# Kernel tuning notes

Measured on AMD Instinct MI355X. Metric: run time of the kernel, lower is better.

Reference implementation:

```python
import jax, jax.numpy as jnp
import numpy as np

B, F, O = 32, 26, 20
IN, G = 2048, 512
REL = 53
EPS = 1e-5  # BatchNorm1d default eps


def setup_inputs() -> dict:
    key = jax.random.key(0)
    ks = jax.random.split(key, 10)
    inp = {
        "region_feats": jax.random.normal(ks[0], (B, F, O, IN), jnp.float32),
        "region_masks": jnp.ones((B, F, O), jnp.float32),
        "rel_feats": jax.random.randint(ks[1], (B, F, O, O), 0, REL, jnp.int64),
        "tem_feats": jax.random.uniform(ks[2], (B, F * O, F * O), jnp.float32),
        # learned params (eval mode: dropout off, BN uses running stats)
        "rel_W": jax.random.normal(ks[3], (G, IN), jnp.float32) * (1.0 / np.sqrt(IN)),
        "rel_b": jnp.zeros((G,), jnp.float32),
        "rel_emb": jax.random.normal(ks[4], (REL, G), jnp.float32) * 0.02,
        "tem_W": jax.random.normal(ks[5], (G, IN), jnp.float32) * (1.0 / np.sqrt(IN)),
        "tem_b": jnp.zeros((G,), jnp.float32),
        "bn_w": jnp.ones((F * O,), jnp.float32),
        "bn_b": jnp.zeros((F * O,), jnp.float32),
        "bn_rm": jnp.zeros((F * O,), jnp.float32),
        "bn_rv": jnp.ones((F * O,), jnp.float32),
    }
    return inp


def reference(region_feats, region_masks, rel_feats, tem_feats,
              rel_W, rel_b, rel_emb, tem_W, tem_b,
              bn_w, bn_b, bn_rm, bn_rv):
    b, f, o, _ = region_feats.shape
    # ---- RELATIONAL FEATURE GRAPH ----
    # [B,F,O,G]
    rel_region = jnp.einsum("bfoi,gi->bfog", region_feats, rel_W) + rel_b
    # embedding lookup: [B,F,O,O,G]
    emb = rel_emb[rel_feats]
    mask = (rel_feats > 0).astype(region_feats.dtype)  # [B,F,O,O]
    msum = jnp.sum(mask, axis=3)                        # [B,F,O]
    # sum_j mask_ij * emb_ij  (masked reduction over neighbor dim)
    emb_sum = jnp.einsum("bfijg,bfij->bfig", emb, mask)
    # sum_j mask_ij * r_i == r_i * msum_i, so (emb_sum + r*msum)/msum
    rel_out = (emb_sum + rel_region * msum[..., None]) / msum[..., None]
    rel_out = rel_out.reshape(b, f * o, -1)
    # ---- TEMPORAL FEATURE GRAPH ----
    tem_region = jnp.einsum("bfoi,gi->bfog", region_feats, tem_W) + tem_b
    tem_region = tem_region.reshape(b, f * o, -1)
    tem_sum = jnp.sum(tem_feats, axis=2)                # [B, F*O]
    tem_out = jnp.matmul(tem_feats, tem_region) / tem_sum[..., None]
    # ---- OUTPUT ----
    out = jnp.concatenate([rel_out, tem_out], axis=-1)  # [B, F*O, 2G]
    out = jnp.tanh(out)
    # BatchNorm1d over channel dim 1 (eval mode, running stats)
    inv = bn_w / jnp.sqrt(bn_rv + EPS)                  # [F*O]
    out = (out - bn_rm[None, :, None]) * inv[None, :, None] + bn_b[None, :, None]
    return out
```

## Files before the change

### kernel.cpp

```cpp
#include <hip/hip_runtime.h>
#include <stdint.h>

#define BB 32
#define FO 520
#define M1 16640
#define KIN 2048
#define KA 2112
#define N1 1024
#define GG 512
#define K2P 576
#define M2 640

typedef unsigned short u16;
typedef short v8s __attribute__((ext_vector_type(8)));
typedef float v4f __attribute__((ext_vector_type(4)));

__device__ __forceinline__ u16 f2bf(float f) {
  union { float f; unsigned u; } v; v.f = f;
  unsigned r = v.u + 0x7fffu + ((v.u >> 16) & 1u);
  return (u16)(r >> 16);
}

__device__ __forceinline__ float fast_tanh(float x) {
  float cx = fminf(fmaxf(x, -15.f), 15.f);
  float e = __expf(2.f * cx);
  return (e - 1.f) / (e + 1.f);
}

__global__ void prep_all_kernel(const float* __restrict__ rf, const int* __restrict__ rel,
                                const float* __restrict__ relW, const float* __restrict__ temW,
                                const float* __restrict__ emb, const float* __restrict__ tem,
                                u16* __restrict__ A1, u16* __restrict__ Wc,
                                u16* __restrict__ A2, float* __restrict__ tsum) {
  const int blk = blockIdx.x;
  const int t = threadIdx.x;
  if (blk < M1 + 1024) {
    const float* src;
    u16* orow;
    if (blk < M1) { src = rf + (size_t)blk * KIN; orow = A1 + (size_t)blk * KA; }
    else {
      const int n = blk - M1;
      src = (n < GG) ? (relW + (size_t)n * KIN) : (temW + (size_t)(n - GG) * KIN);
      orow = Wc + (size_t)n * KA;
    }
    const float4* p = (const float4*)src;
    float4 a = p[2 * t], b = p[2 * t + 1];
    v8s v;
    v[0] = (short)f2bf(a.x); v[1] = (short)f2bf(a.y);
    v[2] = (short)f2bf(a.z); v[3] = (short)f2bf(a.w);
    v[4] = (short)f2bf(b.x); v[5] = (short)f2bf(b.y);
    v[6] = (short)f2bf(b.z); v[7] = (short)f2bf(b.w);
    *(v8s*)(orow + t * 8) = v;
    if (t < 64) {
      float sval = 0.f;
      if (blk < M1) {
        const int* rp = rel + (size_t)blk * 20;
        int cnt = 0, ms = 0;
#pragma unroll
        for (int j = 0; j < 20; ++j) { int ix = rp[j]; cnt += (ix == t + 1); ms += (ix > 0); }
        if (t < 52 && ms > 0) sval = (float)cnt / (float)ms;
      } else {
        const int n = blk - M1;
        if (n < GG && t < 52) sval = emb[(size_t)(t + 1) * GG + n];
      }
      orow[KIN + t] = f2bf(sval);
    }
    return;
  }
  const int w = t >> 6, l = t & 63;
  const int row = (blk - (M1 + 1024)) * 4 + w;
  const int b = row / M2, i = row % M2;
  u16* orow = A2 + (size_t)row * K2P;
  v8s z = {0, 0, 0, 0, 0, 0, 0, 0};
  if (i >= FO) {
    *(v8s*)(orow + l * 8) = z;
    if (l < 8) *(v8s*)(orow + (64 + l) * 8) = z;
    return;
  }
  const float* srow = tem + ((size_t)b * FO + i) * FO;
  float s = 0.f;
  {
    float4 a = *(const float4*)(srow + 8 * l);
    float4 bb = *(const float4*)(srow + 8 * l + 4);
    s += a.x + a.y + a.z + a.w + bb.x + bb.y + bb.z + bb.w;
    v8s v;
    v[0] = (short)f2bf(a.x); v[1] = (short)f2bf(a.y);
    v[2] = (short)f2bf(a.z); v[3] = (short)f2bf(a.w);
    v[4] = (short)f2bf(bb.x); v[5] = (short)f2bf(bb.y);
    v[6] = (short)f2bf(bb.z); v[7] = (short)f2bf(bb.w);
    *(v8s*)(orow + l * 8) = v;
  }
  if (l < 8) {
    if (l == 0) {
      float4 a = *(const float4*)(srow + 512);
      float4 bb = *(const float4*)(srow + 516);
      s += a.x + a.y + a.z + a.w + bb.x + bb.y + bb.z + bb.w;
      v8s v;
      v[0] = (short)f2bf(a.x); v[1] = (short)f2bf(a.y);
      v[2] = (short)f2bf(a.z); v[3] = (short)f2bf(a.w);
      v[4] = (short)f2bf(bb.x); v[5] = (short)f2bf(bb.y);
      v[6] = (short)f2bf(bb.z); v[7] = (short)f2bf(bb.w);
      *(v8s*)(orow + 512) = v;
    } else {
      *(v8s*)(orow + (64 + l) * 8) = z;
    }
  }
#pragma unroll
  for (int off = 32; off > 0; off >>= 1) s += __shfl_down(s, off);
  if (l == 0) tsum[(size_t)b * FO + i] = s;
}

#define G1_STAGE(DST)                                                                            \
  do {                                                                                           \
    u16* dst_ = smem + (DST);                                                                    \
    __builtin_amdgcn_global_load_lds((const __attribute__((address_space(1))) void*)ga0,         \
        (__attribute__((address_space(3))) void*)(dst_ + lofA0), 16, 0, 0);                      \
    __builtin_amdgcn_global_load_lds((const __attribute__((address_space(1))) void*)ga1,         \
        (__attribute__((address_space(3))) void*)(dst_ + lofA1), 16, 0, 0);                      \
    __builtin_amdgcn_global_load_lds((const __attribute__((address_space(1))) void*)gb0,         \
        (__attribute__((address_space(3))) void*)(dst_ + lofB0), 16, 0, 0);                      \
    ga0 += 32; ga1 += 32; gb0 += 32;                                                             \
  } while (0)

#define G1_COMPUTE(CB)                                                                           \
  do {                                                                                           \
    const u16* As_ = smem + (CB) * 12288;                                                        \
    const u16* Bs_ = As_ + 8192;                                                                 \
    v8s af[4], bf[4];                                                                            \
    _Pragma("unroll") for (int t4 = 0; t4 < 4; ++t4) {                                           \
      const int ra = wm * 64 + t4 * 16 + r16;                                                    \
      const int rb = wn * 64 + t4 * 16 + r16;                                                    \
      af[t4] = *(const v8s*)&As_[ra * 32 + ((quad ^ ((ra >> 1) & 3)) * 8)];                      \
      bf[t4] = *(const v8s*)&Bs_[rb * 32 + ((quad ^ ((rb >> 1) & 3)) * 8)];                      \
    }                                                                                            \
    _Pragma("unroll") for (int mtt = 0; mtt < 4; ++mtt)                                          \
      _Pragma("unroll") for (int ntt = 0; ntt < 4; ++ntt)                                        \
        acc[mtt][ntt] =                                                                          \
            __builtin_amdgcn_mfma_f32_16x16x32_bf16(af[mtt], bf[ntt], acc[mtt][ntt], 0, 0, 0);   \
  } while (0)

__global__ __launch_bounds__(512, 4) void gemm1_kernel(
    const u16* __restrict__ A, const u16* __restrict__ Wc,
    const float* __restrict__ rel_b, const float* __restrict__ tem_b,
    const float* __restrict__ bn_w, const float* __restrict__ bn_b,
    const float* __restrict__ bn_rm, const float* __restrict__ bn_rv,
    float* __restrict__ out, u16* __restrict__ BT) {
  __shared__ u16 smem[36864];
  const int tid = threadIdx.x;
  const int lane = tid & 63;
  const int wv = tid >> 6, wm = wv >> 1, wn = wv & 1;
  const int id = blockIdx.x;
  const int wgid = (id & 7) * 65 + (id >> 3);
  const int mt = wgid >> 3, nt = wgid & 7;
  const int m0 = mt * 256, n0 = nt * 128;
  const int quad = lane >> 4, r16 = lane & 15;

  const u16 *ga0, *ga1, *gb0;
  {
    const int r0 = tid >> 2, sl0 = tid & 3;
    ga0 = A + (size_t)(m0 + r0) * KA + (sl0 ^ ((r0 >> 1) & 3)) * 8;
    const int r1 = 128 + (tid >> 2);
    ga1 = A + (size_t)(m0 + r1) * KA + (sl0 ^ ((r1 >> 1) & 3)) * 8;
    gb0 = Wc + (size_t)(n0 + r0) * KA + (sl0 ^ ((r0 >> 1) & 3)) * 8;
  }
  const int lofA0 = wv * 512;
  const int lofA1 = 4096 + wv * 512;
  const int lofB0 = 8192 + wv * 512;

  v4f acc[4][4];
#pragma unroll
  for (int i = 0; i < 4; ++i)
#pragma unroll
    for (int j = 0; j < 4; ++j) { v4f z = {0.f, 0.f, 0.f, 0.f}; acc[i][j] = z; }

  G1_STAGE(0);
  G1_STAGE(12288);

  int cb = 0, nb = 2;
  for (int t = 0; t < 64; ++t) {
    G1_STAGE(nb * 12288);
    asm volatile("s_waitcnt vmcnt(6)" ::: "memory");
    __builtin_amdgcn_s_barrier();
    G1_COMPUTE(cb);
    asm volatile("s_waitcnt lgkmcnt(0)" ::: "memory");
    __builtin_amdgcn_s_barrier();
    cb = (cb == 2) ? 0 : cb + 1;
    nb = (nb == 2) ? 0 : nb + 1;
  }
  {
    const int cb1 = (cb == 2) ? 0 : cb + 1;
    asm volatile("s_waitcnt vmcnt(3)" ::: "memory");
    __builtin_amdgcn_s_barrier();
    G1_COMPUTE(cb);
    asm volatile("s_waitcnt vmcnt(0) lgkmcnt(0)" ::: "memory");
    __builtin_amdgcn_s_barrier();
    G1_COMPUTE(cb1);
  }

  if (n0 < GG) {
#pragma unroll
    for (int mtt = 0; mtt < 4; ++mtt) {
      const int mb = m0 + wm * 64 + mtt * 16 + quad * 4;
      const int bb = mb / FO;
      const int fo0 = mb - bb * FO;
      float inv[4], rm[4], bofs[4];
#pragma unroll
      for (int r = 0; r < 4; ++r) {
        const int fo = fo0 + r;
        inv[r] = bn_w[fo] * rsqrtf(bn_rv[fo] + 1e-5f);
        rm[r] = bn_rm[fo]; bofs[r] = bn_b[fo];
      }
#pragma unroll
      for (int ntt = 0; ntt < 4; ++ntt) {
        const int n = n0 + wn * 64 + ntt * 16 + r16;
        const float rbn = rel_b[n];
#pragma unroll
        for (int r = 0; r < 4; ++r) {
          float val = (fast_tanh(acc[mtt][ntt][r] + rbn) - rm[r]) * inv[r] + bofs[r];
          __builtin_nontemporal_store(val, out + (size_t)(mb + r) * N1 + n);
        }
      }
    }
  } else {
    __syncthreads();
#pragma unroll
    for (int p = 0; p < 2; ++p) {
      if (p) __syncthreads();
      if (wn == p) {
#pragma unroll
        for (int mtt = 0; mtt < 4; ++mtt) {
          const int il = wm * 64 + mtt * 16 + quad * 4;
#pragma unroll
          for (int ntt = 0; ntt < 4; ++ntt) {
            const int gl = ntt * 16 + r16;
            const float tb = tem_b[(n0 - GG) + p * 64 + gl];
            ushort4 w;
            w.x = f2bf(acc[mtt][ntt][0] + tb);
            w.y = f2bf(acc[mtt][ntt][1] + tb);
            w.z = f2bf(acc[mtt][ntt][2] + tb);
            w.w = f2bf(acc[mtt][ntt][3] + tb);
            *(ushort4*)&smem[gl * 264 + il] = w;
          }
        }
      }
      __syncthreads();
#pragma unroll
      for (int pass = 0; pass < 4; ++pass) {
        const int gl = pass * 16 + (tid >> 5);
        const int ch = tid & 31;
        const int m = m0 + ch * 8;
        const int b1 = m / FO;
        const int i1 = m - b1 * FO;
        v8s val = *(const v8s*)&smem[gl * 264 + ch * 8];
        const int g = (n0 - GG) + p * 64 + gl;
        *(v8s*)(BT + ((size_t)(b1 * GG + g)) * K2P + i1) = val;
      }
    }
  }
}

#define G2_STAGE(DST)                                                                            \
  do {                                                                                           \
    u16* dst_ = smem + (DST);                                                                    \
    __builtin_amdgcn_global_load_lds((const __attribute__((address_space(1))) void*)ga0,         \
        (__attribute__((address_space(3))) void*)(dst_ + lofA0), 16, 0, 0);                      \
    __builtin_amdgcn_global_load_lds((const __attribute__((address_space(1))) void*)gb0,         \
        (__attribute__((address_space(3))) void*)(dst_ + lofB0), 16, 0, 0);                      \
    __builtin_amdgcn_global_load_lds((const __attribute__((address_space(1))) void*)ga1,         \
        (__attribute__((address_space(3))) void*)(dst_ + lofA1), 16, 0, 0);                      \
    __builtin_amdgcn_global_load_lds((const __attribute__((address_space(1))) void*)gb1,         \
        (__attribute__((address_space(3))) void*)(dst_ + lofB1), 16, 0, 0);                      \
    ga0 += 32; gb0 += 32; ga1 += 32; gb1 += 32;                                                  \
  } while (0)

#define G2_COMPUTE(CB)                                                                           \
  do {                                                                                           \
    const u16* As_ = smem + (CB) * 8192;                                                         \
    const u16* Bs_ = As_ + 4096;                                                                 \
    v8s af[4], bf[4];                                                                            \
    _Pragma("unroll") for (int t4 = 0; t4 < 4; ++t4) {                                           \
      const int ra = wm * 64 + t4 * 16 + r16;                                                    \
      const int rb = wn * 64 + t4 * 16 + r16;                                                    \
      af[t4] = *(const v8s*)&As_[ra * 32 + ((quad ^ ((ra >> 1) & 3)) * 8)];                      \
      bf[t4] = *(const v8s*)&Bs_[rb * 32 + ((quad ^ ((rb >> 1) & 3)) * 8)];                      \
    }                                                                                            \
    _Pragma("unroll") for (int mtt = 0; mtt < 4; ++mtt)                                          \
      _Pragma("unroll") for (int ntt = 0; ntt < 4; ++ntt)                                        \
        acc[mtt][ntt] =                                                                          \
            __builtin_amdgcn_mfma_f32_16x16x32_bf16(af[mtt], bf[ntt], acc[mtt][ntt], 0, 0, 0);   \
  } while (0)

__global__ __launch_bounds__(256) void gemm2_kernel(
    const u16* __restrict__ A2, const u16* __restrict__ BT,
    const float* __restrict__ tsum,
    const float* __restrict__ bn_w, const float* __restrict__ bn_b,
    const float* __restrict__ bn_rm, const float* __restrict__ bn_rv,
    float* __restrict__ out) {
  __shared__ u16 smem[24576];
  const int tid = threadIdx.x;
  const int lane = tid & 63;
  const int wv = tid >> 6, wm = wv >> 1, wn = wv & 1;
  const int m0 = blockIdx.x * 128;
  const int n0 = blockIdx.y * 128;
  const int b = blockIdx.z;
  const u16* Ab = A2 + (size_t)b * M2 * K2P;
  const u16* Bb = BT + (size_t)b * GG * K2P;
  const int quad = lane >> 4, r16 = lane & 15;

  const u16 *ga0, *ga1, *gb0, *gb1;
  {
    const int r0 = tid >> 2, sl0 = tid & 3;
    const int c0 = sl0 ^ ((r0 >> 1) & 3);
    ga0 = Ab + (size_t)(m0 + r0) * K2P + c0 * 8;
    gb0 = Bb + (size_t)(n0 + r0) * K2P + c0 * 8;
    const int L1 = 256 + tid;
    const int r1 = L1 >> 2, sl1 = L1 & 3;
    const int c1 = sl1 ^ ((r1 >> 1) & 3);
    ga1 = Ab + (size_t)(m0 + r1) * K2P + c1 * 8;
    gb1 = Bb + (size_t)(n0 + r1) * K2P + c1 * 8;
  }
  const int lofA0 = wv * 512, lofA1 = 2048 + wv * 512;
  const int lofB0 = 4096 + wv * 512, lofB1 = 6144 + wv * 512;

  v4f acc[4][4];
#pragma unroll
  for (int i = 0; i < 4; ++i)
#pragma unroll
    for (int j = 0; j < 4; ++j) { v4f z = {0.f, 0.f, 0.f, 0.f}; acc[i][j] = z; }

  G2_STAGE(0);
  G2_STAGE(8192);

  int cb = 0, nb = 2;
  for (int t = 0; t < 16; ++t) {
    G2_STAGE(nb * 8192);
    asm volatile("s_waitcnt vmcnt(8)" ::: "memory");
    __builtin_amdgcn_s_barrier();
    G2_COMPUTE(cb);
    asm volatile("s_waitcnt lgkmcnt(0)" ::: "memory");
    __builtin_amdgcn_s_barrier();
    cb = (cb == 2) ? 0 : cb + 1;
    nb = (nb == 2) ? 0 : nb + 1;
  }
  {
    const int cb1 = (cb == 2) ? 0 : cb + 1;
    asm volatile("s_waitcnt vmcnt(4)" ::: "memory");
    __builtin_amdgcn_s_barrier();
    G2_COMPUTE(cb);
    asm volatile("s_waitcnt vmcnt(0) lgkmcnt(0)" ::: "memory");
    __builtin_amdgcn_s_barrier();
    G2_COMPUTE(cb1);
  }

#pragma unroll
  for (int mtt = 0; mtt < 4; ++mtt) {
    const int ibase = m0 + wm * 64 + mtt * 16 + quad * 4;
    if (ibase >= FO) continue;
    float ts[4], inv[4], rm[4], bofs[4];
#pragma unroll
    for (int r = 0; r < 4; ++r) {
      const int i = ibase + r;
      ts[r] = 1.f / tsum[(size_t)b * FO + i];
      inv[r] = bn_w[i] * rsqrtf(bn_rv[i] + 1e-5f);
      rm[r] = bn_rm[i]; bofs[r] = bn_b[i];
    }
#pragma unroll
    for (int ntt = 0; ntt < 4; ++ntt) {
      const int g = n0 + wn * 64 + ntt * 16 + r16;
#pragma unroll
      for (int r = 0; r < 4; ++r) {
        float val = (fast_tanh(acc[mtt][ntt][r] * ts[r]) - rm[r]) * inv[r] + bofs[r];
        __builtin_nontemporal_store(val, out + ((size_t)(b * FO + (ibase + r))) * N1 + GG + g);
      }
    }
  }
}

extern "C" void kernel_launch(void* const* d_in, const int* in_sizes, int n_in,
                              void* d_out, int out_size, void* d_ws, size_t ws_size,
                              hipStream_t stream) {
  const float* region_feats = (const float*)d_in[0];
  const int* rel_feats = (const int*)d_in[2];
  const float* tem_feats = (const float*)d_in[3];
  const float* rel_W = (const float*)d_in[4];
  const float* rel_b = (const float*)d_in[5];
  const float* rel_emb = (const float*)d_in[6];
  const float* tem_W = (const float*)d_in[7];
  const float* tem_b = (const float*)d_in[8];
  const float* bn_w = (const float*)d_in[9];
  const float* bn_b = (const float*)d_in[10];
  const float* bn_rm = (const float*)d_in[11];
  const float* bn_rv = (const float*)d_in[12];
  float* out = (float*)d_out;

  char* base = (char*)d_ws;
  u16* A1 = (u16*)base;
  u16* Wc = (u16*)(base + 70287360);
  u16* A2 = (u16*)(base + 74612736);
  u16* BT = (u16*)(base + 98205696);
  float* tsum = (float*)(base + 117080064);

  prep_all_kernel<<<M1 + 1024 + 5120, 256, 0, stream>>>(
      region_feats, rel_feats, rel_W, tem_W, rel_emb, tem_feats, A1, Wc, A2, tsum);
  gemm1_kernel<<<520, 512, 0, stream>>>(A1, Wc, rel_b, tem_b,
                                        bn_w, bn_b, bn_rm, bn_rv, out, BT);
  gemm2_kernel<<<dim3(5, 4, 32), 256, 0, stream>>>(A2, BT, tsum,
                                                   bn_w, bn_b, bn_rm, bn_rv, out);
}
```

Measured before the change: 399.6 us.

## Retile gemm1 to 256x256 tiles with split-phase MFMA and tail blocks

The main GEMM now uses 256x256 output tiles, with 8 waves arranged 2x4 and 8x4 MFMA tiles per wave. This raises arithmetic intensity per block and cuts the grid from 520 to 264 blocks, so the whole GEMM fits in about one wave of work across the CUs. The remaining 256 rows are handled by 128x256 tail blocks through a templated body. The K loop interleaves global-to-LDS prefetch with two MFMA half-phases and adds s_setprio and sched_barrier. In exchange, register pressure rises and occupancy drops to 2 blocks per CU, and the tail blocks are unevenly sized.

```diff
diff --git a/kernel.cpp b/kernel.cpp
--- a/kernel.cpp
+++ b/kernel.cpp
@@ -25,6 +25,11 @@
   float cx = fminf(fmaxf(x, -15.f), 15.f);
   float e = __expf(2.f * cx);
   return (e - 1.f) / (e + 1.f);
+}
+
+__device__ __forceinline__ void glds(const u16* g, u16* l) {
+  __builtin_amdgcn_global_load_lds((const __attribute__((address_space(1))) void*)g,
+                                   (__attribute__((address_space(3))) void*)l, 16, 0, 0);
 }
 
 __global__ void prep_all_kernel(const float* __restrict__ rf, const int* __restrict__ rel,
@@ -110,97 +115,123 @@
   if (l == 0) tsum[(size_t)b * FO + i] = s;
 }
 
-#define G1_STAGE(DST)                                                                            \
-  do {                                                                                           \
-    u16* dst_ = smem + (DST);                                                                    \
-    __builtin_amdgcn_global_load_lds((const __attribute__((address_space(1))) void*)ga0,         \
-        (__attribute__((address_space(3))) void*)(dst_ + lofA0), 16, 0, 0);                      \
-    __builtin_amdgcn_global_load_lds((const __attribute__((address_space(1))) void*)ga1,         \
-        (__attribute__((address_space(3))) void*)(dst_ + lofA1), 16, 0, 0);                      \
-    __builtin_amdgcn_global_load_lds((const __attribute__((address_space(1))) void*)gb0,         \
-        (__attribute__((address_space(3))) void*)(dst_ + lofB0), 16, 0, 0);                      \
-    ga0 += 32; ga1 += 32; gb0 += 32;                                                             \
-  } while (0)
-
-#define G1_COMPUTE(CB)                                                                           \
-  do {                                                                                           \
-    const u16* As_ = smem + (CB) * 12288;                                                        \
-    const u16* Bs_ = As_ + 8192;                                                                 \
-    v8s af[4], bf[4];                                                                            \
-    _Pragma("unroll") for (int t4 = 0; t4 < 4; ++t4) {                                           \
-      const int ra = wm * 64 + t4 * 16 + r16;                                                    \
-      const int rb = wn * 64 + t4 * 16 + r16;                                                    \
-      af[t4] = *(const v8s*)&As_[ra * 32 + ((quad ^ ((ra >> 1) & 3)) * 8)];                      \
-      bf[t4] = *(const v8s*)&Bs_[rb * 32 + ((quad ^ ((rb >> 1) & 3)) * 8)];                      \
-    }                                                                                            \
-    _Pragma("unroll") for (int mtt = 0; mtt < 4; ++mtt)                                          \
-      _Pragma("unroll") for (int ntt = 0; ntt < 4; ++ntt)                                        \
-        acc[mtt][ntt] =                                                                          \
-            __builtin_amdgcn_mfma_f32_16x16x32_bf16(af[mtt], bf[ntt], acc[mtt][ntt], 0, 0, 0);   \
-  } while (0)
-
-__global__ __launch_bounds__(512, 4) void gemm1_kernel(
+template <int MR>
+__device__ __forceinline__ void gemm1_body(
     const u16* __restrict__ A, const u16* __restrict__ Wc,
     const float* __restrict__ rel_b, const float* __restrict__ tem_b,
     const float* __restrict__ bn_w, const float* __restrict__ bn_b,
     const float* __restrict__ bn_rm, const float* __restrict__ bn_rv,
-    float* __restrict__ out, u16* __restrict__ BT) {
-  __shared__ u16 smem[36864];
+    float* __restrict__ out, u16* __restrict__ BT, u16* smem,
+    const int m0, const int n0) {
   const int tid = threadIdx.x;
   const int lane = tid & 63;
-  const int wv = tid >> 6, wm = wv >> 1, wn = wv & 1;
-  const int id = blockIdx.x;
-  const int wgid = (id & 7) * 65 + (id >> 3);
-  const int mt = wgid >> 3, nt = wgid & 7;
-  const int m0 = mt * 256, n0 = nt * 128;
+  const int wv = tid >> 6;
+  const int wm = wv >> 2, wn = wv & 3;
   const int quad = lane >> 4, r16 = lane & 15;
-
-  const u16 *ga0, *ga1, *gb0;
-  {
-    const int r0 = tid >> 2, sl0 = tid & 3;
-    ga0 = A + (size_t)(m0 + r0) * KA + (sl0 ^ ((r0 >> 1) & 3)) * 8;
-    const int r1 = 128 + (tid >> 2);
-    ga1 = A + (size_t)(m0 + r1) * KA + (sl0 ^ ((r1 >> 1) & 3)) * 8;
-    gb0 = Wc + (size_t)(n0 + r0) * KA + (sl0 ^ ((r0 >> 1) & 3)) * 8;
-  }
-  const int lofA0 = wv * 512;
-  const int lofA1 = 4096 + wv * 512;
-  const int lofB0 = 8192 + wv * 512;
-
-  v4f acc[4][4];
-#pragma unroll
-  for (int i = 0; i < 4; ++i)
+  constexpr int WM16 = MR * 16;
+  constexpr int L = 2 + MR / 4;
+
+  const int r0 = tid >> 2, sl0 = tid & 3;
+  const int r1 = 128 + r0;
+  const u16* gb0 = Wc + (size_t)(n0 + r0) * KA + (sl0 ^ ((r0 >> 1) & 3)) * 8;
+  const u16* gb1 = Wc + (size_t)(n0 + r1) * KA + (sl0 ^ ((r1 >> 1) & 3)) * 8;
+  const u16* ga0 = A + (size_t)(m0 + r0) * KA + (sl0 ^ ((r0 >> 1) & 3)) * 8;
+  const u16* ga1 = A + (size_t)(m0 + r1) * KA + (sl0 ^ ((r1 >> 1) & 3)) * 8;
+
+  v4f acc[MR][4];
+#pragma unroll
+  for (int i = 0; i < MR; ++i)
 #pragma unroll
     for (int j = 0; j < 4; ++j) { v4f z = {0.f, 0.f, 0.f, 0.f}; acc[i][j] = z; }
 
-  G1_STAGE(0);
-  G1_STAGE(12288);
-
-  int cb = 0, nb = 2;
-  for (int t = 0; t < 64; ++t) {
-    G1_STAGE(nb * 12288);
-    asm volatile("s_waitcnt vmcnt(6)" ::: "memory");
-    __builtin_amdgcn_s_barrier();
-    G1_COMPUTE(cb);
+#pragma unroll
+  for (int pt = 0; pt < 2; ++pt) {
+    u16* d = smem + pt * 16384;
+    glds(gb0, d + 8192 + tid * 8);
+    glds(gb1, d + 12288 + tid * 8);
+    glds(ga0, d + tid * 8);
+    if constexpr (MR == 8) glds(ga1, d + 4096 + tid * 8);
+    gb0 += 32; gb1 += 32; ga0 += 32;
+    if constexpr (MR == 8) ga1 += 32;
+  }
+  if constexpr (MR == 8) asm volatile("s_waitcnt vmcnt(4)" ::: "memory");
+  else                   asm volatile("s_waitcnt vmcnt(3)" ::: "memory");
+  __builtin_amdgcn_s_barrier();
+
+  int cb = 0;
+  for (int t = 0; t < 66; ++t) {
+    const u16* As_ = smem + cb * 16384;
+    const u16* Bs_ = As_ + 8192;
+    const int sb = (cb + 2 >= 3) ? cb - 1 : cb + 2;
+    u16* sd = smem + sb * 16384;
+    v8s af[4], bf[4];
+
+#pragma unroll
+    for (int i = 0; i < 4; ++i) {
+      const int ra = wm * WM16 + i * 16 + r16;
+      af[i] = *(const v8s*)&As_[ra * 32 + ((quad ^ ((ra >> 1) & 3)) * 8)];
+      const int rb = wn * 64 + i * 16 + r16;
+      bf[i] = *(const v8s*)&Bs_[rb * 32 + ((quad ^ ((rb >> 1) & 3)) * 8)];
+    }
+    if (t < 64) {
+      glds(gb0, sd + 8192 + tid * 8);
+      glds(gb1, sd + 12288 + tid * 8);
+      gb0 += 32; gb1 += 32;
+      if constexpr (MR == 4) {
+        glds(ga0, sd + tid * 8);
+        ga0 += 32;
+      }
+    }
+    if constexpr (MR == 4) {
+      if (t < 64) asm volatile("s_waitcnt vmcnt(3)" ::: "memory");
+      else        asm volatile("s_waitcnt vmcnt(0)" ::: "memory");
+    }
+    __builtin_amdgcn_s_barrier();
     asm volatile("s_waitcnt lgkmcnt(0)" ::: "memory");
-    __builtin_amdgcn_s_barrier();
+    __builtin_amdgcn_sched_barrier(0);
+    __builtin_amdgcn_s_setprio(1);
+#pragma unroll
+    for (int i = 0; i < 4; ++i)
+#pragma unroll
+      for (int j = 0; j < 4; ++j)
+        acc[i][j] = __builtin_amdgcn_mfma_f32_16x16x32_bf16(af[i], bf[j], acc[i][j], 0, 0, 0);
+    __builtin_amdgcn_s_setprio(0);
+    __builtin_amdgcn_s_barrier();
+
+    if constexpr (MR == 8) {
+#pragma unroll
+      for (int i = 0; i < 4; ++i) {
+        const int ra = wm * WM16 + (4 + i) * 16 + r16;
+        af[i] = *(const v8s*)&As_[ra * 32 + ((quad ^ ((ra >> 1) & 3)) * 8)];
+      }
+      if (t < 64) {
+        glds(ga0, sd + tid * 8);
+        glds(ga1, sd + 4096 + tid * 8);
+        ga0 += 32; ga1 += 32;
+        asm volatile("s_waitcnt vmcnt(4)" ::: "memory");
+      } else {
+        asm volatile("s_waitcnt vmcnt(0)" ::: "memory");
+      }
+      __builtin_amdgcn_s_barrier();
+      asm volatile("s_waitcnt lgkmcnt(0)" ::: "memory");
+      __builtin_amdgcn_sched_barrier(0);
+      __builtin_amdgcn_s_setprio(1);
+#pragma unroll
+      for (int i = 0; i < 4; ++i)
+#pragma unroll
+        for (int j = 0; j < 4; ++j)
+          acc[4 + i][j] = __builtin_amdgcn_mfma_f32_16x16x32_bf16(af[i], bf[j], acc[4 + i][j], 0, 0, 0);
+      __builtin_amdgcn_s_setprio(0);
+      __builtin_amdgcn_s_barrier();
+    }
+
     cb = (cb == 2) ? 0 : cb + 1;
-    nb = (nb == 2) ? 0 : nb + 1;
-  }
-  {
-    const int cb1 = (cb == 2) ? 0 : cb + 1;
-    asm volatile("s_waitcnt vmcnt(3)" ::: "memory");
-    __builtin_amdgcn_s_barrier();
-    G1_COMPUTE(cb);
-    asm volatile("s_waitcnt vmcnt(0) lgkmcnt(0)" ::: "memory");
-    __builtin_amdgcn_s_barrier();
-    G1_COMPUTE(cb1);
   }
 
   if (n0 < GG) {
 #pragma unroll
-    for (int mtt = 0; mtt < 4; ++mtt) {
-      const int mb = m0 + wm * 64 + mtt * 16 + quad * 4;
+    for (int mtt = 0; mtt < MR; ++mtt) {
+      const int mb = m0 + wm * WM16 + mtt * 16 + quad * 4;
       const int bb = mb / FO;
       const int fo0 = mb - bb * FO;
       float inv[4], rm[4], bofs[4];
@@ -222,14 +253,15 @@
       }
     }
   } else {
+    constexpr int SP = MR * 32 + 8;
     __syncthreads();
 #pragma unroll
-    for (int p = 0; p < 2; ++p) {
+    for (int p = 0; p < 4; ++p) {
       if (p) __syncthreads();
       if (wn == p) {
 #pragma unroll
-        for (int mtt = 0; mtt < 4; ++mtt) {
-          const int il = wm * 64 + mtt * 16 + quad * 4;
+        for (int mtt = 0; mtt < MR; ++mtt) {
+          const int il = wm * WM16 + mtt * 16 + quad * 4;
 #pragma unroll
           for (int ntt = 0; ntt < 4; ++ntt) {
             const int gl = ntt * 16 + r16;
@@ -239,37 +271,64 @@
             w.y = f2bf(acc[mtt][ntt][1] + tb);
             w.z = f2bf(acc[mtt][ntt][2] + tb);
             w.w = f2bf(acc[mtt][ntt][3] + tb);
-            *(ushort4*)&smem[gl * 264 + il] = w;
+            *(ushort4*)&smem[gl * SP + il] = w;
           }
         }
       }
       __syncthreads();
-#pragma unroll
-      for (int pass = 0; pass < 4; ++pass) {
-        const int gl = pass * 16 + (tid >> 5);
-        const int ch = tid & 31;
-        const int m = m0 + ch * 8;
-        const int b1 = m / FO;
-        const int i1 = m - b1 * FO;
-        v8s val = *(const v8s*)&smem[gl * 264 + ch * 8];
-        const int g = (n0 - GG) + p * 64 + gl;
-        *(v8s*)(BT + ((size_t)(b1 * GG + g)) * K2P + i1) = val;
-      }
-    }
+      if constexpr (MR == 8) {
+#pragma unroll
+        for (int sp = 0; sp < 4; ++sp) {
+          const int gl = sp * 16 + (tid >> 5);
+          const int ch = tid & 31;
+          const int m = m0 + ch * 8;
+          const int b1 = m / FO;
+          const int i1 = m - b1 * FO;
+          v8s val = *(const v8s*)&smem[gl * SP + ch * 8];
+          const int g = (n0 - GG) + p * 64 + gl;
+          *(v8s*)(BT + ((size_t)(b1 * GG + g)) * K2P + i1) = val;
+        }
+      } else {
+#pragma unroll
+        for (int sp = 0; sp < 2; ++sp) {
+          const int gl = sp * 32 + (tid >> 4);
+          const int ch = tid & 15;
+          const int m = m0 + ch * 8;
+          const int b1 = m / FO;
+          const int i1 = m - b1 * FO;
+          v8s val = *(const v8s*)&smem[gl * SP + ch * 8];
+          const int g = (n0 - GG) + p * 64 + gl;
+          *(v8s*)(BT + ((size_t)(b1 * GG + g)) * K2P + i1) = val;
+        }
+      }
+    }
+  }
+}
+
+__global__ __launch_bounds__(512, 2) void gemm1_kernel(
+    const u16* __restrict__ A, const u16* __restrict__ Wc,
+    const float* __restrict__ rel_b, const float* __restrict__ tem_b,
+    const float* __restrict__ bn_w, const float* __restrict__ bn_b,
+    const float* __restrict__ bn_rm, const float* __restrict__ bn_rv,
+    float* __restrict__ out, u16* __restrict__ BT) {
+  __shared__ u16 smem[49152];
+  const int id = blockIdx.x;
+  if (id < 256) {
+    const int wgid = (id & 7) * 32 + (id >> 3);
+    const int m0 = (wgid >> 2) * 256, n0 = (wgid & 3) * 256;
+    gemm1_body<8>(A, Wc, rel_b, tem_b, bn_w, bn_b, bn_rm, bn_rv, out, BT, smem, m0, n0);
+  } else {
+    const int sid = id - 256;
+    const int m0 = 16384 + (sid >> 2) * 128, n0 = (sid & 3) * 256;
+    gemm1_body<4>(A, Wc, rel_b, tem_b, bn_w, bn_b, bn_rm, bn_rv, out, BT, smem, m0, n0);
   }
 }
 
 #define G2_STAGE(DST)                                                                            \
   do {                                                                                           \
     u16* dst_ = smem + (DST);                                                                    \
-    __builtin_amdgcn_global_load_lds((const __attribute__((address_space(1))) void*)ga0,         \
-        (__attribute__((address_space(3))) void*)(dst_ + lofA0), 16, 0, 0);                      \
-    __builtin_amdgcn_global_load_lds((const __attribute__((address_space(1))) void*)gb0,         \
-        (__attribute__((address_space(3))) void*)(dst_ + lofB0), 16, 0, 0);                      \
-    __builtin_amdgcn_global_load_lds((const __attribute__((address_space(1))) void*)ga1,         \
-        (__attribute__((address_space(3))) void*)(dst_ + lofA1), 16, 0, 0);                      \
-    __builtin_amdgcn_global_load_lds((const __attribute__((address_space(1))) void*)gb1,         \
-        (__attribute__((address_space(3))) void*)(dst_ + lofB1), 16, 0, 0);                      \
+    glds(ga0, dst_ + lofA0); glds(gb0, dst_ + lofB0);                                            \
+    glds(ga1, dst_ + lofA1); glds(gb1, dst_ + lofB1);                                            \
     ga0 += 32; gb0 += 32; ga1 += 32; gb1 += 32;                                                  \
   } while (0)
 
@@ -402,7 +461,7 @@
 
   prep_all_kernel<<<M1 + 1024 + 5120, 256, 0, stream>>>(
       region_feats, rel_feats, rel_W, tem_W, rel_emb, tem_feats, A1, Wc, A2, tsum);
-  gemm1_kernel<<<520, 512, 0, stream>>>(A1, Wc, rel_b, tem_b,
+  gemm1_kernel<<<264, 512, 0, stream>>>(A1, Wc, rel_b, tem_b,
                                         bn_w, bn_b, bn_rm, bn_rv, out, BT);
   gemm2_kernel<<<dim3(5, 4, 32), 256, 0, stream>>>(A2, BT, tsum,
                                                    bn_w, bn_b, bn_rm, bn_rv, out);
```

Measured after the change: 409.9 us. 1.03x slower.
